# Kernel tuning notes

Measured on AMD Instinct MI355X. Metric: run time of the kernel, lower is better.

Reference implementation:

```python
import jax, jax.numpy as jnp
import numpy as np
from jax import lax


def _conv(x, w, b, stride, pad):
    # x: NCHW, w: OIHW (pytorch Conv2d layout)
    y = lax.conv_general_dilated(x, w, window_strides=(stride, stride),
                                 padding=((pad, pad), (pad, pad)),
                                 dimension_numbers=('NCHW', 'OIHW', 'NCHW'))
    return y + b[None, :, None, None]


def _deconv(x, w, b):
    # PyTorch ConvTranspose2d(k=4, stride=2, padding=1); w: [in, out, 4, 4]
    # Equivalent to conv with lhs_dilation=2, padding k-1-p=2, flipped/transposed kernel.
    wk = jnp.flip(w, (2, 3)).transpose(1, 0, 2, 3)  # -> OIHW
    y = lax.conv_general_dilated(x, wk, window_strides=(1, 1),
                                 padding=((2, 2), (2, 2)), lhs_dilation=(2, 2),
                                 dimension_numbers=('NCHW', 'OIHW', 'NCHW'))
    return y + b[None, :, None, None]


def _mse(a, b):
    d = a - b
    return jnp.mean(d * d)


def _forward(x, enc_w1, enc_b1, enc_w2, enc_b2, enc_w3, enc_b3, codebook,
             dec_w1, dec_b1, dec_w2, dec_b2, dec_w3, dec_b3, beta=0.25):
    # ---- Encoder ----
    h = jax.nn.relu(_conv(x, enc_w1, enc_b1, 2, 1))
    h = jax.nn.relu(_conv(h, enc_w2, enc_b2, 2, 1))
    z_e = _conv(h, enc_w3, enc_b3, 1, 1)            # [B, D, H, W]
    B, D, H, W = z_e.shape

    # ---- Vector quantize ----
    z_flat = z_e.transpose(0, 2, 3, 1).reshape(-1, D)              # [N, D]
    dist = (jnp.sum(z_flat * z_flat, axis=1, keepdims=True)
            + jnp.sum(codebook * codebook, axis=1)
            - 2.0 * z_flat @ codebook.T)                            # [N, K]
    idx = jnp.argmin(dist, axis=1)                                  # [N]
    z_q = codebook[idx].reshape(B, H, W, D).transpose(0, 3, 1, 2)   # [B, D, H, W]

    commitment_loss = beta * _mse(lax.stop_gradient(z_e), z_q)
    codebook_loss = _mse(z_e, lax.stop_gradient(z_q))
    vq_loss = codebook_loss + commitment_loss
    z_q_st = z_e + lax.stop_gradient(z_q - z_e)     # straight-through

    # ---- Decoder ----
    d1 = jax.nn.relu(_deconv(z_q_st, dec_w1, dec_b1))
    d2 = jax.nn.relu(_deconv(d1, dec_w2, dec_b2))
    x_recon = _conv(d2, dec_w3, dec_b3, 1, 1)

    recon_loss = _mse(x_recon, x)
    total_loss = recon_loss + vq_loss
    return x_recon, total_loss, recon_loss, vq_loss


def setup_inputs() -> dict:
    key = jax.random.key(0)
    ks = jax.random.split(key, 16)
    s = 0.05
    K, D, Hc = 512, 64, 128
    return {
        'x':       jax.random.normal(ks[0], (64, 3, 128, 128), jnp.float32),
        'enc_w1':  jax.random.normal(ks[1], (Hc, 3, 4, 4), jnp.float32) * s,
        'enc_b1':  jnp.zeros((Hc,), jnp.float32),
        'enc_w2':  jax.random.normal(ks[2], (Hc, Hc, 4, 4), jnp.float32) * s,
        'enc_b2':  jnp.zeros((Hc,), jnp.float32),
        'enc_w3':  jax.random.normal(ks[3], (D, Hc, 3, 3), jnp.float32) * s,
        'enc_b3':  jnp.zeros((D,), jnp.float32),
        'codebook': jax.random.uniform(ks[4], (K, D), jnp.float32, -1.0 / K, 1.0 / K),
        'dec_w1':  jax.random.normal(ks[5], (D, Hc, 4, 4), jnp.float32) * s,  # ConvTranspose [in,out,k,k]
        'dec_b1':  jnp.zeros((Hc,), jnp.float32),
        'dec_w2':  jax.random.normal(ks[6], (Hc, Hc, 4, 4), jnp.float32) * s,
        'dec_b2':  jnp.zeros((Hc,), jnp.float32),
        'dec_w3':  jax.random.normal(ks[7], (3, Hc, 3, 3), jnp.float32) * s,
        'dec_b3':  jnp.zeros((3,), jnp.float32),
    }


def reference(x, enc_w1, enc_b1, enc_w2, enc_b2, enc_w3, enc_b3, codebook,
              dec_w1, dec_b1, dec_w2, dec_b2, dec_w3, dec_b3):
    return _forward(x, enc_w1, enc_b1, enc_w2, enc_b2, enc_w3, enc_b3, codebook,
                    dec_w1, dec_b1, dec_w2, dec_b2, dec_w3, dec_b3)
```

## Files before the change

kernel.cpp:

```cpp
#include <hip/hip_runtime.h>
#include <hip/hip_bf16.h>


typedef __attribute__((ext_vector_type(8))) short short8;
typedef __attribute__((ext_vector_type(16))) float f32x16;
typedef __attribute__((ext_vector_type(4))) float f32x4;

__device__ __forceinline__ unsigned short f2bf(float f) {
  union { __hip_bfloat16 b; unsigned short u; } cv;
  cv.b = __float2bfloat16(f);
  return cv.u;
}
__device__ __forceinline__ unsigned pack2bf(float a, float b) {
  return (unsigned)f2bf(a) | ((unsigned)f2bf(b) << 16);
}

template<int CI, int NTAP, int NTALL>
__global__ void repack_conv_w(const float* __restrict__ w,
                              unsigned short* __restrict__ wb, int co_real) {
  const int KC = CI / 16;
  const int total = NTAP * KC * NTALL * 512;
  int i = blockIdx.x * 256 + threadIdx.x;
  if (i >= total) return;
  int j = i & 7, lane = (i >> 3) & 63, t2 = i >> 9;
  int nt = t2 % NTALL; t2 /= NTALL;
  int kc = t2 % KC; int tap = t2 / KC;
  int co = nt * 32 + (lane & 31);
  int ci = kc * 16 + (lane >> 5) * 8 + j;
  float v = (co < co_real) ? w[(co * CI + ci) * NTAP + tap] : 0.f;
  wb[i] = f2bf(v);
}

template<int CI, int CO, int NTALL>
__global__ void repack_deconv_w(const float* __restrict__ w,
                                unsigned short* __restrict__ wb) {
  const int KC = CI / 16;
  const int total = 16 * KC * NTALL * 512;
  int i = blockIdx.x * 256 + threadIdx.x;
  if (i >= total) return;
  int j = i & 7, lane = (i >> 3) & 63, t2 = i >> 9;
  int nt = t2 % NTALL; t2 /= NTALL;
  int kc = t2 % KC; t2 /= KC;
  int tap = t2 & 3, cls = t2 >> 2;
  int a = cls >> 1, b = cls & 1, ti = tap >> 1, tj = tap & 1;
  int kh = 2 * ti + 1 - a, kw = 2 * tj + 1 - b;
  int co = nt * 32 + (lane & 31);
  int ci = kc * 16 + (lane >> 5) * 8 + j;
  wb[i] = f2bf(w[((ci * CO + co) * 4 + kh) * 4 + kw]);
}

__global__ void repack_conv4_w(const float* __restrict__ w,
                               unsigned short* __restrict__ wb) {
  const int total = 9 * 4 * 512;
  int i = blockIdx.x * 256 + threadIdx.x;
  if (i >= total) return;
  int j = i & 7, lane = (i >> 3) & 63, tk = i >> 9;
  int kc = tk & 3, t = tk >> 2;
  int co = lane & 15;
  int ci = kc * 32 + (lane >> 4) * 8 + j;
  float v = (co < 3) ? w[(co * 128 + ci) * 9 + t] : 0.f;
  wb[i] = f2bf(v);
}

__global__ void repack_conv1_w(const float* __restrict__ w,
                               float* __restrict__ wc1) {
  int i = blockIdx.x * 256 + threadIdx.x;
  if (i >= 6144) return;
  int tap = i >> 7, co = i & 127;
  wc1[i] = w[co * 48 + tap];
}

__global__ void repack_cb(const float* __restrict__ cb,
                          unsigned short* __restrict__ cbf) {
  int i = blockIdx.x * 256 + threadIdx.x;
  int j = i & 7, lane = (i >> 3) & 63;
  int kc = (i >> 9) & 3, tile = i >> 11;
  int code = tile * 32 + (lane & 31);
  int d = kc * 16 + (lane >> 5) * 8 + j;
  cbf[i] = f2bf(cb[code * 64 + d]);
}
__global__ void cnorm_k(const float* __restrict__ cb, float* __restrict__ cn) {
  int k = blockIdx.x * 256 + threadIdx.x;
  if (k >= 512) return;
  const float4* r = (const float4*)(cb + k * 64);
  float s = 0.f;
  #pragma unroll
  for (int q = 0; q < 16; ++q) {
    float4 v = r[q];
    s = fmaf(v.x, v.x, s); s = fmaf(v.y, v.y, s);
    s = fmaf(v.z, v.z, s); s = fmaf(v.w, v.w, s);
  }
  cn[k] = s;
}

__global__ __launch_bounds__(256, 4) void conv1_k(
    const float* __restrict__ x, const float* __restrict__ wc1,
    const float* __restrict__ bias, unsigned short* __restrict__ out) {
  __shared__ float swc[6144];
  __shared__ float sx[3 * 10 * 132];
  int tid = threadIdx.x;
  int n = blockIdx.x >> 4, ohq = blockIdx.x & 15;
  #pragma unroll
  for (int q = 0; q < 6; ++q) {
    int i = (q * 256 + tid) * 4;
    *(float4*)&swc[i] = *(const float4*)&wc1[i];
  }
  int ihb = 8 * ohq - 1;
  for (int i = tid; i < 3960; i += 256) {
    int ci = i / 1320, rem = i - ci * 1320;
    int r = rem / 132, c = rem - r * 132;
    int ih = ihb + r, iw = c - 1;
    float v = 0.f;
    if ((unsigned)ih < 128u && (unsigned)iw < 128u)
      v = x[(n * 3 + ci) * 16384 + ih * 128 + iw];
    sx[i] = v;
  }
  __syncthreads();
  int ow = tid >> 2, cg = tid & 3;
  #pragma unroll
  for (int cob = 0; cob < 2; ++cob) {
    int co0 = cob * 64 + cg * 16;
    float4 acc[4][4];
    float4 bq[4];
    #pragma unroll
    for (int q = 0; q < 4; ++q) bq[q] = *(const float4*)&bias[co0 + q * 4];
    #pragma unroll
    for (int o = 0; o < 4; ++o)
      #pragma unroll
      for (int q = 0; q < 4; ++q) acc[o][q] = bq[q];
    for (int ci = 0; ci < 3; ++ci)
      for (int kh = 0; kh < 4; ++kh) {
        #pragma unroll
        for (int kw = 0; kw < 4; ++kw) {
          int tap = ci * 16 + kh * 4 + kw;
          const float* wp = &swc[tap * 128 + co0];
          float4 w0 = *(const float4*)(wp);
          float4 w1 = *(const float4*)(wp + 4);
          float4 w2 = *(const float4*)(wp + 8);
          float4 w3 = *(const float4*)(wp + 12);
          const float* xp = &sx[ci * 1320 + kh * 132 + 2 * ow + kw];
          #pragma unroll
          for (int o = 0; o < 4; ++o) {
            float xv = xp[o * 264];
            acc[o][0].x = fmaf(xv, w0.x, acc[o][0].x);
            acc[o][0].y = fmaf(xv, w0.y, acc[o][0].y);
            acc[o][0].z = fmaf(xv, w0.z, acc[o][0].z);
            acc[o][0].w = fmaf(xv, w0.w, acc[o][0].w);
            acc[o][1].x = fmaf(xv, w1.x, acc[o][1].x);
            acc[o][1].y = fmaf(xv, w1.y, acc[o][1].y);
            acc[o][1].z = fmaf(xv, w1.z, acc[o][1].z);
            acc[o][1].w = fmaf(xv, w1.w, acc[o][1].w);
            acc[o][2].x = fmaf(xv, w2.x, acc[o][2].x);
            acc[o][2].y = fmaf(xv, w2.y, acc[o][2].y);
            acc[o][2].z = fmaf(xv, w2.z, acc[o][2].z);
            acc[o][2].w = fmaf(xv, w2.w, acc[o][2].w);
            acc[o][3].x = fmaf(xv, w3.x, acc[o][3].x);
            acc[o][3].y = fmaf(xv, w3.y, acc[o][3].y);
            acc[o][3].z = fmaf(xv, w3.z, acc[o][3].z);
            acc[o][3].w = fmaf(xv, w3.w, acc[o][3].w);
          }
        }
      }
    #pragma unroll
    for (int o = 0; o < 4; ++o) {
      int oh = ohq * 4 + o;
      unsigned short* op = out + ((size_t)(n * 64 + oh) * 64 + ow) * 128 + co0;
      uint4 u0, u1;
      u0.x = pack2bf(fmaxf(acc[o][0].x, 0.f), fmaxf(acc[o][0].y, 0.f));
      u0.y = pack2bf(fmaxf(acc[o][0].z, 0.f), fmaxf(acc[o][0].w, 0.f));
      u0.z = pack2bf(fmaxf(acc[o][1].x, 0.f), fmaxf(acc[o][1].y, 0.f));
      u0.w = pack2bf(fmaxf(acc[o][1].z, 0.f), fmaxf(acc[o][1].w, 0.f));
      u1.x = pack2bf(fmaxf(acc[o][2].x, 0.f), fmaxf(acc[o][2].y, 0.f));
      u1.y = pack2bf(fmaxf(acc[o][2].z, 0.f), fmaxf(acc[o][2].w, 0.f));
      u1.z = pack2bf(fmaxf(acc[o][3].x, 0.f), fmaxf(acc[o][3].y, 0.f));
      u1.w = pack2bf(fmaxf(acc[o][3].z, 0.f), fmaxf(acc[o][3].w, 0.f));
      *(uint4*)(op) = u0;
      *(uint4*)(op + 8) = u1;
    }
  }
}

template<int CI, int CO, int NTALL, int NT, int S, int IH, int IW, int OH, int OW,
         int NTAP, int KW, int STRIDE, bool DECONV, bool RELU, bool F32OUT>
__global__ __launch_bounds__(256, 2) void mconv_k(
    const unsigned short* __restrict__ in, const unsigned short* __restrict__ wb,
    const float* __restrict__ bias, void* __restrict__ outv,
    const unsigned short* __restrict__ zeropg) {
  const int KC = CI / 16;
  const int TSZ = KC * NT * 512;
  const int STG = KC * NT / 4;
  __shared__ unsigned short sB[2][TSZ];
  int tid = threadIdx.x, lane = tid & 63, wv = tid >> 6;
  int m0 = blockIdx.x * (128 * S) + wv * (32 * S);
  int cls = DECONV ? blockIdx.y : 0;
  int cog = blockIdx.z;
  int ca = cls >> 1, cb2 = cls & 1;
  int khalf = lane >> 5;
  int n_[S], oh_[S], ow_[S];
  #pragma unroll
  for (int s = 0; s < S; ++s) {
    int mm = m0 + s * 32 + (lane & 31);
    n_[s] = mm / (OH * OW);
    int rem = mm % (OH * OW);
    oh_[s] = rem / OW; ow_[s] = rem % OW;
  }
  f32x16 acc[S][NT];
  #pragma unroll
  for (int s = 0; s < S; ++s)
    #pragma unroll
    for (int t = 0; t < NT; ++t)
      #pragma unroll
      for (int e = 0; e < 16; ++e) acc[s][t][e] = 0.f;

  const unsigned short* wcls = wb + (size_t)cls * NTAP * KC * NTALL * 512;
  uint4 st[STG];
  #pragma unroll
  for (int q = 0; q < STG; ++q) {
    int i = q * 256 + tid;
    int kc = i / (NT * 64), r = i - kc * (NT * 64);
    st[q] = *(const uint4*)(wcls + (size_t)(kc * NTALL + cog * NT) * 512 + r * 8);
  }
  #pragma unroll
  for (int q = 0; q < STG; ++q) {
    int i = q * 256 + tid;
    *(uint4*)&sB[0][i * 8] = st[q];
  }
  __syncthreads();

  for (int t = 0; t < NTAP; ++t) {
    int cur = t & 1;
    if (t + 1 < NTAP) {
      const unsigned short* wt = wcls + (size_t)(t + 1) * KC * NTALL * 512;
      #pragma unroll
      for (int q = 0; q < STG; ++q) {
        int i = q * 256 + tid;
        int kc = i / (NT * 64), r = i - kc * (NT * 64);
        st[q] = *(const uint4*)(wt + (size_t)(kc * NTALL + cog * NT) * 512 + r * 8);
      }
    }
    const unsigned short* ap[S];
    #pragma unroll
    for (int s = 0; s < S; ++s) {
      int ih, iw;
      if (DECONV) { ih = oh_[s] + ca - (t >> 1); iw = ow_[s] + cb2 - (t & 1); }
      else        { ih = STRIDE * oh_[s] - 1 + t / KW; iw = STRIDE * ow_[s] - 1 + t % KW; }
      bool valid = ((unsigned)ih < (unsigned)IH) && ((unsigned)iw < (unsigned)IW);
      ap[s] = valid ? (in + ((size_t)(n_[s] * IH + ih) * IW + iw) * CI + khalf * 8)
                    : (zeropg + khalf * 8);
    }
    #pragma unroll
    for (int kc = 0; kc < KC; ++kc) {
      short8 a[S];
      #pragma unroll
      for (int s = 0; s < S; ++s) a[s] = *(const short8*)(ap[s] + kc * 16);
      #pragma unroll
      for (int nt = 0; nt < NT; ++nt) {
        short8 b = *(const short8*)&sB[cur][(kc * NT + nt) * 512 + lane * 8];
        #pragma unroll
        for (int s = 0; s < S; ++s)
          acc[s][nt] = __builtin_amdgcn_mfma_f32_32x32x16_bf16(a[s], b, acc[s][nt], 0, 0, 0);
      }
    }
    if (t + 1 < NTAP) {
      #pragma unroll
      for (int q = 0; q < STG; ++q) {
        int i = q * 256 + tid;
        *(uint4*)&sB[cur ^ 1][i * 8] = st[q];
      }
    }
    __syncthreads();
  }

  int col = lane & 31;
  #pragma unroll
  for (int s = 0; s < S; ++s)
    #pragma unroll
    for (int nt = 0; nt < NT; ++nt) {
      int co = (cog * NT + nt) * 32 + col;
      float bv = bias[co];
      #pragma unroll
      for (int r = 0; r < 16; ++r) {
        int mrow = (r & 3) + 8 * (r >> 2) + 4 * khalf;
        int mp = m0 + s * 32 + mrow;
        int n2 = mp / (OH * OW), r2 = mp % (OH * OW);
        int oh2 = r2 / OW, ow2 = r2 % OW;
        float v = acc[s][nt][r] + bv;
        if (RELU) v = fmaxf(v, 0.f);
        size_t idx;
        if (DECONV)
          idx = ((size_t)(n2 * (2 * OH) + 2 * oh2 + ca) * (2 * OW) + 2 * ow2 + cb2) * CO + co;
        else
          idx = ((size_t)(n2 * OH + oh2) * OW + ow2) * CO + co;
        if (F32OUT) ((float*)outv)[idx] = v;
        else        ((unsigned short*)outv)[idx] = f2bf(v);
      }
    }
}

__global__ __launch_bounds__(256, 2) void vq2_k(
    const float* __restrict__ ze, const float* __restrict__ cb,
    const unsigned short* __restrict__ cbf, const float* __restrict__ cnorm,
    unsigned short* __restrict__ zq, float* __restrict__ acc_loss) {
  __shared__ unsigned short sC[16384];
  __shared__ int s_idx[4][32];
  int tid = threadIdx.x, lane = tid & 63, wv = tid >> 6;
  int m0 = blockIdx.x * 128 + wv * 32;
  int col = lane & 31, khalf = lane >> 5;
  const float* zrow = ze + (size_t)(m0 + col) * 64 + khalf * 8;
  short8 af[4];
  #pragma unroll
  for (int kc = 0; kc < 4; ++kc) {
    float4 a = *(const float4*)(zrow + kc * 16);
    float4 b = *(const float4*)(zrow + kc * 16 + 4);
    short8 f;
    f[0] = (short)f2bf(a.x); f[1] = (short)f2bf(a.y);
    f[2] = (short)f2bf(a.z); f[3] = (short)f2bf(a.w);
    f[4] = (short)f2bf(b.x); f[5] = (short)f2bf(b.y);
    f[6] = (short)f2bf(b.z); f[7] = (short)f2bf(b.w);
    af[kc] = f;
  }
  float best[16]; int bidx[16];
  #pragma unroll
  for (int r = 0; r < 16; ++r) { best[r] = 3.4e38f; bidx[r] = 0; }
  for (int half = 0; half < 2; ++half) {
    #pragma unroll
    for (int q = 0; q < 8; ++q) {
      int i = q * 256 + tid;
      *(uint4*)&sC[i * 8] = *(const uint4*)(cbf + half * 16384 + i * 8);
    }
    __syncthreads();
    #pragma unroll
    for (int t8 = 0; t8 < 8; ++t8) {
      int tt = half * 8 + t8;
      f32x16 acc;
      #pragma unroll
      for (int e = 0; e < 16; ++e) acc[e] = 0.f;
      #pragma unroll
      for (int kc = 0; kc < 4; ++kc) {
        short8 bf_ = *(const short8*)&sC[(t8 * 4 + kc) * 512 + lane * 8];
        acc = __builtin_amdgcn_mfma_f32_32x32x16_bf16(af[kc], bf_, acc, 0, 0, 0);
      }
      float cn = cnorm[tt * 32 + col];
      int code = tt * 32 + col;
      #pragma unroll
      for (int r = 0; r < 16; ++r) {
        float d = fmaf(-2.f, acc[r], cn);
        if (d < best[r]) { best[r] = d; bidx[r] = code; }
      }
    }
    __syncthreads();
  }
  #pragma unroll
  for (int off = 1; off < 32; off <<= 1) {
    #pragma unroll
    for (int r = 0; r < 16; ++r) {
      float ob = __shfl_xor(best[r], off, 64);
      int   oi = __shfl_xor(bidx[r], off, 64);
      if (ob < best[r]) { best[r] = ob; bidx[r] = oi; }
    }
  }
  if (col == 0) {
    #pragma unroll
    for (int r = 0; r < 16; ++r)
      s_idx[wv][(r & 3) + 8 * (r >> 2) + 4 * khalf] = bidx[r];
  }
  __syncthreads();
  int row = lane >> 1, half2 = lane & 1;
  int m = m0 + row;
  int idx = s_idx[wv][row];
  const float4* crow = (const float4*)(cb + idx * 64 + half2 * 32);
  const float4* zp = (const float4*)(ze + (size_t)m * 64 + half2 * 32);
  uint2* zqp = (uint2*)(zq + (size_t)m * 64 + half2 * 32);
  float lsum = 0.f;
  #pragma unroll
  for (int q = 0; q < 8; ++q) {
    float4 c4 = crow[q];
    float4 z4 = zp[q];
    uint2 u; u.x = pack2bf(c4.x, c4.y); u.y = pack2bf(c4.z, c4.w);
    zqp[q] = u;
    float d;
    d = z4.x - c4.x; lsum = fmaf(d, d, lsum);
    d = z4.y - c4.y; lsum = fmaf(d, d, lsum);
    d = z4.z - c4.z; lsum = fmaf(d, d, lsum);
    d = z4.w - c4.w; lsum = fmaf(d, d, lsum);
  }
  #pragma unroll
  for (int off = 32; off > 0; off >>= 1) lsum += __shfl_down(lsum, off, 64);
  if (lane == 0) atomicAdd(acc_loss, lsum);
}

__global__ __launch_bounds__(256, 2) void conv4_k(
    const unsigned short* __restrict__ in, const unsigned short* __restrict__ wb,
    const float* __restrict__ bias, const float* __restrict__ x,
    float* __restrict__ out, float* __restrict__ acc_loss,
    const unsigned short* __restrict__ zeropg) {
  __shared__ unsigned short sW[18432];
  int tid = threadIdx.x, lane = tid & 63, wv = tid >> 6;
  #pragma unroll
  for (int q = 0; q < 9; ++q) {
    int i = q * 256 + tid;
    *(uint4*)&sW[i * 8] = *(const uint4*)(wb + i * 8);
  }
  int m0 = blockIdx.x * 256 + wv * 64;
  int quad = lane >> 4, mloc = lane & 15;
  int n_[4], oh_[4], ow_[4];
  #pragma unroll
  for (int s = 0; s < 4; ++s) {
    int mm = m0 + s * 16 + mloc;
    n_[s] = mm >> 14;
    int rem = mm & 16383;
    oh_[s] = rem >> 7; ow_[s] = rem & 127;
  }
  f32x4 acc[4];
  #pragma unroll
  for (int s = 0; s < 4; ++s)
    #pragma unroll
    for (int e = 0; e < 4; ++e) acc[s][e] = 0.f;
  __syncthreads();
  #pragma unroll
  for (int t = 0; t < 9; ++t) {
    int dh = t / 3 - 1, dw = t % 3 - 1;
    const unsigned short* ap[4];
    #pragma unroll
    for (int s = 0; s < 4; ++s) {
      int ih = oh_[s] + dh, iw = ow_[s] + dw;
      bool valid = ((unsigned)ih < 128u) && ((unsigned)iw < 128u);
      ap[s] = valid ? (in + ((size_t)(n_[s] * 128 + ih) * 128 + iw) * 128 + quad * 8)
                    : (zeropg + quad * 8);
    }
    #pragma unroll
    for (int kc = 0; kc < 4; ++kc) {
      short8 bf_ = *(const short8*)&sW[(t * 4 + kc) * 512 + lane * 8];
      #pragma unroll
      for (int s = 0; s < 4; ++s) {
        short8 a = *(const short8*)(ap[s] + kc * 32);
        acc[s] = __builtin_amdgcn_mfma_f32_16x16x32_bf16(a, bf_, acc[s], 0, 0, 0);
      }
    }
  }
  int co = lane & 15;
  float bv = (co < 3) ? bias[co] : 0.f;
  float lsum = 0.f;
  #pragma unroll
  for (int s = 0; s < 4; ++s)
    #pragma unroll
    for (int r = 0; r < 4; ++r) {
      int m = m0 + s * 16 + quad * 4 + r;
      if (co < 3) {
        float v = acc[s][r] + bv;
        int n2 = m >> 14, r2 = m & 16383;
        int gi = (n2 * 3 + co) * 16384 + r2;
        out[gi] = v;
        float d = v - x[gi];
        lsum = fmaf(d, d, lsum);
      }
    }
  #pragma unroll
  for (int off = 32; off > 0; off >>= 1) lsum += __shfl_down(lsum, off, 64);
  if (lane == 0) atomicAdd(acc_loss, lsum);
}

__global__ void finalize_k(const float* __restrict__ accv, float* __restrict__ out) {
  if (threadIdx.x == 0 && blockIdx.x == 0) {
    float recon = accv[0] / 3145728.0f;
    float vq = 1.25f * accv[1] / 4194304.0f;
    out[3145728] = recon + vq;
    out[3145729] = recon;
    out[3145730] = vq;
  }
}

extern "C" void kernel_launch(void* const* d_in, const int* in_sizes, int n_in,
                              void* d_out, int out_size, void* d_ws, size_t ws_size,
                              hipStream_t stream) {
  const float* x   = (const float*)d_in[0];
  const float* ew1 = (const float*)d_in[1];
  const float* eb1 = (const float*)d_in[2];
  const float* ew2 = (const float*)d_in[3];
  const float* eb2 = (const float*)d_in[4];
  const float* ew3 = (const float*)d_in[5];
  const float* eb3 = (const float*)d_in[6];
  const float* cb  = (const float*)d_in[7];
  const float* dw1 = (const float*)d_in[8];
  const float* db1 = (const float*)d_in[9];
  const float* dw2 = (const float*)d_in[10];
  const float* db2 = (const float*)d_in[11];
  const float* dw3 = (const float*)d_in[12];
  const float* db3 = (const float*)d_in[13];
  float* out = (float*)d_out;

  char* ws = (char*)d_ws;
  float* acc = (float*)ws;
  unsigned short* zeropg = (unsigned short*)(ws + 256);
  char* p = ws + 1024;
  unsigned short* wb2  = (unsigned short*)p; p += 524288;
  unsigned short* wb3  = (unsigned short*)p; p += 147456;
  unsigned short* wb4  = (unsigned short*)p; p += 36864;
  unsigned short* wbd1 = (unsigned short*)p; p += 262144;
  unsigned short* wbd2 = (unsigned short*)p; p += 524288;
  unsigned short* cbf  = (unsigned short*)p; p += 65536;
  float*          cnrm = (float*)p;          p += 2048;
  float*          wc1  = (float*)p;          p += 24576;
  size_t fixed = (size_t)(p - ws);

  unsigned short* h1 = (unsigned short*)p; p += 67108864ull;
  unsigned short* h2 = (unsigned short*)p; p += 16777216ull;
  float*          ze = (float*)p;          p += 16777216ull;
  unsigned short* zq = (unsigned short*)p; p += 8388608ull;
  unsigned short* d2 = (unsigned short*)p;
  size_t base = fixed + 67108864ull + 16777216ull + 16777216ull + 8388608ull;
  int CD = 64;
  while (CD > 1 && base + (size_t)CD * 4194304ull > ws_size) CD >>= 1;

  hipMemsetAsync(ws, 0, 1024, stream);
  repack_conv_w<128, 16, 4><<<(16 * 8 * 4 * 512 + 255) / 256, 256, 0, stream>>>(ew2, wb2, 128);
  repack_conv_w<128, 9, 2><<<(9 * 8 * 2 * 512 + 255) / 256, 256, 0, stream>>>(ew3, wb3, 64);
  repack_conv4_w<<<(9 * 4 * 512 + 255) / 256, 256, 0, stream>>>(dw3, wb4);
  repack_deconv_w<64, 128, 4><<<(16 * 4 * 4 * 512 + 255) / 256, 256, 0, stream>>>(dw1, wbd1);
  repack_deconv_w<128, 128, 4><<<(16 * 8 * 4 * 512 + 255) / 256, 256, 0, stream>>>(dw2, wbd2);
  repack_cb<<<128, 256, 0, stream>>>(cb, cbf);
  cnorm_k<<<2, 256, 0, stream>>>(cb, cnrm);
  repack_conv1_w<<<24, 256, 0, stream>>>(ew1, wc1);

  conv1_k<<<1024, 256, 0, stream>>>(x, wc1, eb1, h1);
  mconv_k<128, 128, 4, 2, 4, 64, 64, 32, 32, 16, 4, 2, false, true, false>
      <<<dim3(128, 1, 2), 256, 0, stream>>>(h1, wb2, eb2, h2, zeropg);
  mconv_k<128, 64, 2, 2, 2, 32, 32, 32, 32, 9, 3, 1, false, false, true>
      <<<dim3(256, 1, 1), 256, 0, stream>>>(h2, wb3, eb3, ze, zeropg);
  vq2_k<<<512, 256, 0, stream>>>(ze, cb, cbf, cnrm, zq, acc + 1);
  mconv_k<64, 128, 4, 2, 4, 32, 32, 32, 32, 4, 2, 1, true, true, false>
      <<<dim3(128, 4, 2), 256, 0, stream>>>(zq, wbd1, db1, h1, zeropg);

  for (int n0 = 0; n0 < 64; n0 += CD) {
    const unsigned short* d1c = h1 + (size_t)n0 * 524288;
    mconv_k<128, 128, 4, 2, 4, 64, 64, 64, 64, 4, 2, 1, true, true, false>
        <<<dim3(CD * 8, 4, 2), 256, 0, stream>>>(d1c, wbd2, db2, d2, zeropg);
    conv4_k<<<CD * 64, 256, 0, stream>>>(d2, wb4, db3, x + (size_t)n0 * 49152,
                                         out + (size_t)n0 * 49152, acc, zeropg);
  }
  finalize_k<<<1, 64, 0, stream>>>(acc, out);
}
```

Measured before the change: 1.103 ms.

## Cover all output channels and deconv parity classes per block; enlarge conv4 tile

The generic MFMA conv kernel now computes all output channels in one block (NT equals the full channel count). Each input fragment is therefore loaded once instead of once per channel group, and weight staging becomes a plain contiguous copy. For the transposed convolutions, the four output parity classes are looped inside one block, with a per-class epilogue and accumulator reset, instead of being spread over grid.y and grid.z. The final 3-channel conv handles 8 row tiles per wave instead of 4. The trade-off is fewer blocks, which lowers occupancy (one decoder layer drops to 256 blocks), plus larger LDS and staging-register footprints.

Result: slower. 1.361 ms (+23.4%).

```diff
diff --git a/kernel.cpp b/kernel.cpp
--- a/kernel.cpp
+++ b/kernel.cpp
@@ -180,8 +180,8 @@
   }
 }
 
-template<int CI, int CO, int NTALL, int NT, int S, int IH, int IW, int OH, int OW,
-         int NTAP, int KW, int STRIDE, bool DECONV, bool RELU, bool F32OUT>
+template<int CI, int CO, int NT, int S, int IH, int IW, int OH, int OW,
+         int NTAP, int KW, int STRIDE, int NCLS, bool RELU, bool F32OUT>
 __global__ __launch_bounds__(256, 2) void mconv_k(
     const unsigned short* __restrict__ in, const unsigned short* __restrict__ wb,
     const float* __restrict__ bias, void* __restrict__ outv,
@@ -189,12 +189,11 @@
   const int KC = CI / 16;
   const int TSZ = KC * NT * 512;
   const int STG = KC * NT / 4;
+  const int TT = NCLS * NTAP;
+  const bool DECONV = (NCLS > 1);
   __shared__ unsigned short sB[2][TSZ];
   int tid = threadIdx.x, lane = tid & 63, wv = tid >> 6;
-  int m0 = blockIdx.x * (128 * S) + wv * (32 * S);
-  int cls = DECONV ? blockIdx.y : 0;
-  int cog = blockIdx.z;
-  int ca = cls >> 1, cb2 = cls & 1;
+  int m0 = blockIdx.x * (4 * S * 32) + wv * (32 * S);
   int khalf = lane >> 5;
   int n_[S], oh_[S], ow_[S];
   #pragma unroll
@@ -212,38 +211,33 @@
       #pragma unroll
       for (int e = 0; e < 16; ++e) acc[s][t][e] = 0.f;
 
-  const unsigned short* wcls = wb + (size_t)cls * NTAP * KC * NTALL * 512;
   uint4 st[STG];
   #pragma unroll
-  for (int q = 0; q < STG; ++q) {
-    int i = q * 256 + tid;
-    int kc = i / (NT * 64), r = i - kc * (NT * 64);
-    st[q] = *(const uint4*)(wcls + (size_t)(kc * NTALL + cog * NT) * 512 + r * 8);
-  }
-  #pragma unroll
-  for (int q = 0; q < STG; ++q) {
-    int i = q * 256 + tid;
-    *(uint4*)&sB[0][i * 8] = st[q];
-  }
+  for (int q = 0; q < STG; ++q)
+    st[q] = *(const uint4*)(wb + (q * 256 + tid) * 8);
+  #pragma unroll
+  for (int q = 0; q < STG; ++q)
+    *(uint4*)&sB[0][(q * 256 + tid) * 8] = st[q];
   __syncthreads();
 
-  for (int t = 0; t < NTAP; ++t) {
-    int cur = t & 1;
-    if (t + 1 < NTAP) {
-      const unsigned short* wt = wcls + (size_t)(t + 1) * KC * NTALL * 512;
-      #pragma unroll
-      for (int q = 0; q < STG; ++q) {
-        int i = q * 256 + tid;
-        int kc = i / (NT * 64), r = i - kc * (NT * 64);
-        st[q] = *(const uint4*)(wt + (size_t)(kc * NTALL + cog * NT) * 512 + r * 8);
-      }
+  int col = lane & 31;
+  for (int tt = 0; tt < TT; ++tt) {
+    int cur = tt & 1;
+    int cls = DECONV ? (tt / NTAP) : 0;
+    int tap = DECONV ? (tt % NTAP) : tt;
+    int ca = cls >> 1, cb2 = cls & 1;
+    if (tt + 1 < TT) {
+      const unsigned short* wt = wb + (size_t)(tt + 1) * TSZ;
+      #pragma unroll
+      for (int q = 0; q < STG; ++q)
+        st[q] = *(const uint4*)(wt + (q * 256 + tid) * 8);
     }
     const unsigned short* ap[S];
     #pragma unroll
     for (int s = 0; s < S; ++s) {
       int ih, iw;
-      if (DECONV) { ih = oh_[s] + ca - (t >> 1); iw = ow_[s] + cb2 - (t & 1); }
-      else        { ih = STRIDE * oh_[s] - 1 + t / KW; iw = STRIDE * ow_[s] - 1 + t % KW; }
+      if (DECONV) { ih = oh_[s] + ca - (tap >> 1); iw = ow_[s] + cb2 - (tap & 1); }
+      else        { ih = STRIDE * oh_[s] - 1 + tap / KW; iw = STRIDE * ow_[s] - 1 + tap % KW; }
       bool valid = ((unsigned)ih < (unsigned)IH) && ((unsigned)iw < (unsigned)IW);
       ap[s] = valid ? (in + ((size_t)(n_[s] * IH + ih) * IW + iw) * CI + khalf * 8)
                     : (zeropg + khalf * 8);
@@ -261,40 +255,57 @@
           acc[s][nt] = __builtin_amdgcn_mfma_f32_32x32x16_bf16(a[s], b, acc[s][nt], 0, 0, 0);
       }
     }
-    if (t + 1 < NTAP) {
-      #pragma unroll
-      for (int q = 0; q < STG; ++q) {
-        int i = q * 256 + tid;
-        *(uint4*)&sB[cur ^ 1][i * 8] = st[q];
-      }
+    if (tt + 1 < TT) {
+      #pragma unroll
+      for (int q = 0; q < STG; ++q)
+        *(uint4*)&sB[cur ^ 1][(q * 256 + tid) * 8] = st[q];
+    }
+    if (DECONV && tap == NTAP - 1) {
+      #pragma unroll
+      for (int s = 0; s < S; ++s)
+        #pragma unroll
+        for (int nt = 0; nt < NT; ++nt) {
+          int co = nt * 32 + col;
+          float bv = bias[co];
+          #pragma unroll
+          for (int r = 0; r < 16; ++r) {
+            int mrow = (r & 3) + 8 * (r >> 2) + 4 * khalf;
+            int mp = m0 + s * 32 + mrow;
+            int n2 = mp / (OH * OW), r2 = mp % (OH * OW);
+            int oh2 = r2 / OW, ow2 = r2 % OW;
+            float v = acc[s][nt][r] + bv;
+            if (RELU) v = fmaxf(v, 0.f);
+            size_t idx = ((size_t)(n2 * (2 * OH) + 2 * oh2 + ca) * (2 * OW) + 2 * ow2 + cb2) * CO + co;
+            if (F32OUT) ((float*)outv)[idx] = v;
+            else        ((unsigned short*)outv)[idx] = f2bf(v);
+            acc[s][nt][r] = 0.f;
+          }
+        }
     }
     __syncthreads();
   }
 
-  int col = lane & 31;
-  #pragma unroll
-  for (int s = 0; s < S; ++s)
-    #pragma unroll
-    for (int nt = 0; nt < NT; ++nt) {
-      int co = (cog * NT + nt) * 32 + col;
-      float bv = bias[co];
-      #pragma unroll
-      for (int r = 0; r < 16; ++r) {
-        int mrow = (r & 3) + 8 * (r >> 2) + 4 * khalf;
-        int mp = m0 + s * 32 + mrow;
-        int n2 = mp / (OH * OW), r2 = mp % (OH * OW);
-        int oh2 = r2 / OW, ow2 = r2 % OW;
-        float v = acc[s][nt][r] + bv;
-        if (RELU) v = fmaxf(v, 0.f);
-        size_t idx;
-        if (DECONV)
-          idx = ((size_t)(n2 * (2 * OH) + 2 * oh2 + ca) * (2 * OW) + 2 * ow2 + cb2) * CO + co;
-        else
-          idx = ((size_t)(n2 * OH + oh2) * OW + ow2) * CO + co;
-        if (F32OUT) ((float*)outv)[idx] = v;
-        else        ((unsigned short*)outv)[idx] = f2bf(v);
-      }
-    }
+  if (!DECONV) {
+    #pragma unroll
+    for (int s = 0; s < S; ++s)
+      #pragma unroll
+      for (int nt = 0; nt < NT; ++nt) {
+        int co = nt * 32 + col;
+        float bv = bias[co];
+        #pragma unroll
+        for (int r = 0; r < 16; ++r) {
+          int mrow = (r & 3) + 8 * (r >> 2) + 4 * khalf;
+          int mp = m0 + s * 32 + mrow;
+          int n2 = mp / (OH * OW), r2 = mp % (OH * OW);
+          int oh2 = r2 / OW, ow2 = r2 % OW;
+          float v = acc[s][nt][r] + bv;
+          if (RELU) v = fmaxf(v, 0.f);
+          size_t idx = ((size_t)(n2 * OH + oh2) * OW + ow2) * CO + co;
+          if (F32OUT) ((float*)outv)[idx] = v;
+          else        ((unsigned short*)outv)[idx] = f2bf(v);
+        }
+      }
+  }
 }
 
 __global__ __launch_bounds__(256, 2) void vq2_k(
@@ -401,28 +412,28 @@
     int i = q * 256 + tid;
     *(uint4*)&sW[i * 8] = *(const uint4*)(wb + i * 8);
   }
-  int m0 = blockIdx.x * 256 + wv * 64;
+  int m0 = blockIdx.x * 512 + wv * 128;
   int quad = lane >> 4, mloc = lane & 15;
-  int n_[4], oh_[4], ow_[4];
-  #pragma unroll
-  for (int s = 0; s < 4; ++s) {
+  int n_[8], oh_[8], ow_[8];
+  #pragma unroll
+  for (int s = 0; s < 8; ++s) {
     int mm = m0 + s * 16 + mloc;
     n_[s] = mm >> 14;
     int rem = mm & 16383;
     oh_[s] = rem >> 7; ow_[s] = rem & 127;
   }
-  f32x4 acc[4];
-  #pragma unroll
-  for (int s = 0; s < 4; ++s)
+  f32x4 acc[8];
+  #pragma unroll
+  for (int s = 0; s < 8; ++s)
     #pragma unroll
     for (int e = 0; e < 4; ++e) acc[s][e] = 0.f;
   __syncthreads();
   #pragma unroll
   for (int t = 0; t < 9; ++t) {
     int dh = t / 3 - 1, dw = t % 3 - 1;
-    const unsigned short* ap[4];
-    #pragma unroll
-    for (int s = 0; s < 4; ++s) {
+    const unsigned short* ap[8];
+    #pragma unroll
+    for (int s = 0; s < 8; ++s) {
       int ih = oh_[s] + dh, iw = ow_[s] + dw;
       bool valid = ((unsigned)ih < 128u) && ((unsigned)iw < 128u);
       ap[s] = valid ? (in + ((size_t)(n_[s] * 128 + ih) * 128 + iw) * 128 + quad * 8)
@@ -432,7 +443,7 @@
     for (int kc = 0; kc < 4; ++kc) {
       short8 bf_ = *(const short8*)&sW[(t * 4 + kc) * 512 + lane * 8];
       #pragma unroll
-      for (int s = 0; s < 4; ++s) {
+      for (int s = 0; s < 8; ++s) {
         short8 a = *(const short8*)(ap[s] + kc * 32);
         acc[s] = __builtin_amdgcn_mfma_f32_16x16x32_bf16(a, bf_, acc[s], 0, 0, 0);
       }
@@ -442,7 +453,7 @@
   float bv = (co < 3) ? bias[co] : 0.f;
   float lsum = 0.f;
   #pragma unroll
-  for (int s = 0; s < 4; ++s)
+  for (int s = 0; s < 8; ++s)
     #pragma unroll
     for (int r = 0; r < 4; ++r) {
       int m = m0 + s * 16 + quad * 4 + r;
@@ -523,19 +534,19 @@
   repack_conv1_w<<<24, 256, 0, stream>>>(ew1, wc1);
 
   conv1_k<<<1024, 256, 0, stream>>>(x, wc1, eb1, h1);
-  mconv_k<128, 128, 4, 2, 4, 64, 64, 32, 32, 16, 4, 2, false, true, false>
-      <<<dim3(128, 1, 2), 256, 0, stream>>>(h1, wb2, eb2, h2, zeropg);
-  mconv_k<128, 64, 2, 2, 2, 32, 32, 32, 32, 9, 3, 1, false, false, true>
-      <<<dim3(256, 1, 1), 256, 0, stream>>>(h2, wb3, eb3, ze, zeropg);
+  mconv_k<128, 128, 4, 2, 64, 64, 32, 32, 16, 4, 2, 1, true, false>
+      <<<256, 256, 0, stream>>>(h1, wb2, eb2, h2, zeropg);
+  mconv_k<128, 64, 2, 2, 32, 32, 32, 32, 9, 3, 1, 1, false, true>
+      <<<256, 256, 0, stream>>>(h2, wb3, eb3, ze, zeropg);
   vq2_k<<<512, 256, 0, stream>>>(ze, cb, cbf, cnrm, zq, acc + 1);
-  mconv_k<64, 128, 4, 2, 4, 32, 32, 32, 32, 4, 2, 1, true, true, false>
-      <<<dim3(128, 4, 2), 256, 0, stream>>>(zq, wbd1, db1, h1, zeropg);
+  mconv_k<64, 128, 4, 2, 32, 32, 32, 32, 4, 2, 1, 4, true, false>
+      <<<256, 256, 0, stream>>>(zq, wbd1, db1, h1, zeropg);
 
   for (int n0 = 0; n0 < 64; n0 += CD) {
     const unsigned short* d1c = h1 + (size_t)n0 * 524288;
-    mconv_k<128, 128, 4, 2, 4, 64, 64, 64, 64, 4, 2, 1, true, true, false>
-        <<<dim3(CD * 8, 4, 2), 256, 0, stream>>>(d1c, wbd2, db2, d2, zeropg);
-    conv4_k<<<CD * 64, 256, 0, stream>>>(d2, wb4, db3, x + (size_t)n0 * 49152,
+    mconv_k<128, 128, 4, 2, 64, 64, 64, 64, 4, 2, 1, 4, true, false>
+        <<<CD * 16, 256, 0, stream>>>(d1c, wbd2, db2, d2, zeropg);
+    conv4_k<<<CD * 32, 256, 0, stream>>>(d2, wb4, db3, x + (size_t)n0 * 49152,
                                          out + (size_t)n0 * 49152, acc, zeropg);
   }
   finalize_k<<<1, 64, 0, stream>>>(acc, out);
```
